# Performance work log

Measured on AMD Instinct MI355X. Metric: run time of the kernel, lower is better.

The kernel has to match this reference:

```python
import jax, jax.numpy as jnp
import numpy as np

N_BITS = 8
IN_F = 4096
OUT_F = 1024
THRESHOLD = 0.5


def _ripple_accumulate(bits, n_bits):
    # bits: [N, I, n_bits], little-endian bit vectors (last bit is the sign bit).
    # Sequentially add each of the I bit-vectors into an accumulator via
    # ripple-carry binary addition (straight-through gradients on the carry).
    N = bits.shape[0]
    dt = bits.dtype

    def add_step(acc, x):  # acc, x: [N, n_bits]
        carry = jnp.zeros((N,), dt)
        outs = []
        for b in range(n_bits):
            s = acc[:, b] + x[:, b] + carry
            carry = jax.lax.stop_gradient(jnp.floor(s * 0.5))
            outs.append(s - 2.0 * carry)  # s mod 2, STE through the floor
        return jnp.stack(outs, axis=-1), None

    acc0 = jnp.zeros((N, n_bits), dt)
    acc, _ = jax.lax.scan(add_step, acc0, jnp.swapaxes(bits, 0, 1))  # scan over I
    return acc


def residual_adder(features, weights, true_sum, n_bits):
    # features/weights/true_sum: [N, I, n_bits]. Ripple-carry accumulate the
    # filtered feature bits per neuron, return the bitwise residual vs the
    # target sum bits (trigger signal).
    acc = _ripple_accumulate(features, n_bits)  # [N, n_bits]
    return acc - true_sum[:, 0, :]


def setup_inputs() -> dict:
    key = jax.random.key(0)
    k1, k2, k3 = jax.random.split(key, 3)
    latent = jax.random.uniform(k1, (1, IN_F), dtype=jnp.float32)
    true_sum = jax.random.randint(k2, (1, OUT_F * N_BITS), 0, 2).astype(jnp.float32)
    weight = jax.random.uniform(k3, (IN_F, OUT_F * N_BITS), dtype=jnp.float32)
    return {"latent": latent, "true_sum": true_sum, "weight": weight}


def reference(latent, true_sum, weight):
    B = latent.shape[0]  # must be 1 (see torch repeat semantics)
    dt = weight.dtype
    # straight-through hard binarization of the weight
    hard = weight + jax.lax.stop_gradient((weight > THRESHOLD).astype(dt) - weight)
    powers = (2.0 ** jnp.arange(N_BITS, dtype=dt)).at[-1].multiply(-1.0)  # two's complement
    int_w = jax.lax.stop_gradient((hard.reshape(IN_F, OUT_F, N_BITS) * powers).sum(-1))  # [IN_F, OUT_F]
    int_s = jax.lax.stop_gradient((true_sum.reshape(B, OUT_F, N_BITS) * powers).sum(-1))  # [B, OUT_F]
    pred = latent @ int_w  # [B, OUT_F]
    loss = 0.5 * jnp.mean((pred - int_s) ** 2)
    # per-bit filtered features, regrouped per neuron
    filtered = jax.lax.stop_gradient(latent)[:, :, None] * hard[None]  # [B, IN_F, OUT_F*N_BITS]
    fbn = filtered.reshape(B, IN_F, OUT_F, N_BITS).transpose(0, 2, 1, 3).reshape(B * OUT_F, IN_F, N_BITS)
    # torch 2D .repeat(1, IN_F, 1) -> [1, B*IN_F, OUT_F*N_BITS]
    ts = jnp.tile(true_sum[None], (1, IN_F, 1))
    tbn = ts.reshape(1, B * IN_F, OUT_F, N_BITS).transpose(0, 2, 1, 3).reshape(OUT_F, B * IN_F, N_BITS)
    wbn = jnp.broadcast_to(weight[None], (B, IN_F, OUT_F * N_BITS)).reshape(B, IN_F, OUT_F, N_BITS).transpose(0, 2, 1, 3).reshape(B * OUT_F, IN_F, N_BITS)
    trigger = residual_adder(fbn, wbn, tbn, N_BITS)  # [B*OUT_F, N_BITS]
    return loss, trigger
```

## Files before the change

kernel.cpp:

```cpp
#include <hip/hip_runtime.h>
#include <cmath>

#define IN_F   4096
#define OUT_F  1024
#define NBITS  8
#define JTOT   (OUT_F * NBITS)
#define TB     256
#define CPT    4
#define JBLK   (TB * CPT)
#define NJB    (JTOT / JBLK)
#define ROWS   64
#define NCHUNK (IN_F / ROWS)

typedef float f32x4 __attribute__((ext_vector_type(4)));

__global__ __launch_bounds__(TB) void colsum_kernel(
    const float* __restrict__ w, const float* __restrict__ latent,
    float* __restrict__ partials, float* __restrict__ out) {
  const int j0 = (blockIdx.x * TB + threadIdx.x) * CPT;
  const int chunk = blockIdx.y;
  const int i0 = chunk * ROWS;
  if (blockIdx.x == 0 && blockIdx.y == 0 && threadIdx.x == 0) out[0] = 0.0f;

  float a0 = 0.f, a1 = 0.f, a2 = 0.f, a3 = 0.f;
  const f32x4* wp = reinterpret_cast<const f32x4*>(w + (size_t)i0 * JTOT + j0);
#pragma unroll 32
  for (int r = 0; r < ROWS; ++r) {
    const float lat = latent[i0 + r];
    const f32x4 v = __builtin_nontemporal_load(wp + (size_t)r * (JTOT / 4));
    a0 += (v.x > 0.5f) ? lat : 0.0f;
    a1 += (v.y > 0.5f) ? lat : 0.0f;
    a2 += (v.z > 0.5f) ? lat : 0.0f;
    a3 += (v.w > 0.5f) ? lat : 0.0f;
  }
  float* p = partials + (size_t)chunk * JTOT + j0;
  p[0] = a0; p[1] = a1; p[2] = a2; p[3] = a3;
}

__global__ __launch_bounds__(TB) void finalize_kernel(
    const float* __restrict__ partials, const float* __restrict__ true_sum,
    float* __restrict__ out) {
  const int tid = threadIdx.x;
  const int j = blockIdx.x * TB + tid;
  double s = 0.0;
#pragma unroll 8
  for (int c = 0; c < NCHUNK; ++c)
    s += (double)partials[(size_t)c * JTOT + j];

  __shared__ double S[TB];
  __shared__ double err[TB / NBITS];
  S[tid] = s;
  __syncthreads();

  if (tid < TB / NBITS) {
    const int o_local = tid;
    const int jbase = blockIdx.x * TB + o_local * NBITS;
    const double pw[NBITS] = {1.0, 2.0, 4.0, 8.0, 16.0, 32.0, 64.0, -128.0};
    double C = 0.0, pred = 0.0, ints = 0.0;
#pragma unroll
    for (int b = 0; b < NBITS; ++b) {
      const double Sb = S[o_local * NBITS + b];
      const double ts = (double)true_sum[jbase + b];
      const double T  = Sb + C;
      const double c2 = floor(T * 0.5);
      const double ab = T - 2.0 * c2;
      C = c2;
      out[1 + jbase + b] = (float)(ab - ts);
      pred += pw[b] * Sb;
      ints += pw[b] * ts;
    }
    const double d = pred - ints;
    err[o_local] = d * d;
  }
  __syncthreads();

  if (tid == 0) {
    double e = 0.0;
    for (int k = 0; k < TB / NBITS; ++k) e += err[k];
    atomicAdd(out, (float)(e * (0.5 / (double)OUT_F)));
  }
}

extern "C" void kernel_launch(void* const* d_in, const int* in_sizes, int n_in,
                              void* d_out, int out_size, void* d_ws, size_t ws_size,
                              hipStream_t stream) {
  const float* latent   = (const float*)d_in[0];
  const float* true_sum = (const float*)d_in[1];
  const float* w        = (const float*)d_in[2];
  float* out = (float*)d_out;
  float* partials = (float*)d_ws;

  colsum_kernel<<<dim3(NJB, NCHUNK), TB, 0, stream>>>(w, latent, partials, out);
  finalize_kernel<<<dim3(JTOT / TB), TB, 0, stream>>>(partials, true_sum, out);
}
```

Measured before the change: 192.6 us.

## Fuse column-sum and finalize into one kernel via last-block atomic counters

Merges the two kernels into one: each column block's chunk writes its partials, and the last chunk to finish (found with an atomic counter) reduces all partials for that column block and computes the ripple bits and the loss. A second counter lets the last finalizer sum the per-block losses deterministically instead of using a float atomicAdd. This removes one kernel launch and the gap between the launches, but adds a memset launch, threadfences, and a tail in which 8 blocks do the reduction serially.

```diff
diff --git a/kernel.cpp b/kernel.cpp
--- a/kernel.cpp
+++ b/kernel.cpp
@@ -11,16 +11,20 @@
 #define NJB    (JTOT / JBLK)
 #define ROWS   64
 #define NCHUNK (IN_F / ROWS)
+#define NEUR_PER_CB (JBLK / NBITS)
 
 typedef float f32x4 __attribute__((ext_vector_type(4)));
 
-__global__ __launch_bounds__(TB) void colsum_kernel(
+__global__ __launch_bounds__(TB) void fused_kernel(
     const float* __restrict__ w, const float* __restrict__ latent,
-    float* __restrict__ partials, float* __restrict__ out) {
-  const int j0 = (blockIdx.x * TB + threadIdx.x) * CPT;
+    const float* __restrict__ true_sum, float* __restrict__ partials,
+    double* __restrict__ lossp, int* __restrict__ ctr,
+    int* __restrict__ fin_ctr, float* __restrict__ out) {
+  const int x = blockIdx.x;
   const int chunk = blockIdx.y;
+  const int tid = threadIdx.x;
+  const int j0 = x * JBLK + tid * CPT;
   const int i0 = chunk * ROWS;
-  if (blockIdx.x == 0 && blockIdx.y == 0 && threadIdx.x == 0) out[0] = 0.0f;
 
   float a0 = 0.f, a1 = 0.f, a2 = 0.f, a3 = 0.f;
   const f32x4* wp = reinterpret_cast<const f32x4*>(w + (size_t)i0 * JTOT + j0);
@@ -33,51 +37,65 @@
     a2 += (v.z > 0.5f) ? lat : 0.0f;
     a3 += (v.w > 0.5f) ? lat : 0.0f;
   }
-  float* p = partials + (size_t)chunk * JTOT + j0;
-  p[0] = a0; p[1] = a1; p[2] = a2; p[3] = a3;
-}
+  f32x4 acc = {a0, a1, a2, a3};
+  *reinterpret_cast<f32x4*>(partials + (size_t)chunk * JTOT + j0) = acc;
 
-__global__ __launch_bounds__(TB) void finalize_kernel(
-    const float* __restrict__ partials, const float* __restrict__ true_sum,
-    float* __restrict__ out) {
-  const int tid = threadIdx.x;
-  const int j = blockIdx.x * TB + tid;
-  double s = 0.0;
+  __threadfence();
+  __syncthreads();
+  __shared__ int is_last;
+  if (tid == 0)
+    is_last = (atomicAdd(ctr + x, 1) == NCHUNK - 1) ? 1 : 0;
+  __syncthreads();
+  if (!is_last) return;
+  __threadfence();
+
+  double s0 = 0.0, s1 = 0.0, s2 = 0.0, s3 = 0.0;
+  const float* pp = partials + j0;
 #pragma unroll 8
-  for (int c = 0; c < NCHUNK; ++c)
-    s += (double)partials[(size_t)c * JTOT + j];
-
-  __shared__ double S[TB];
-  __shared__ double err[TB / NBITS];
-  S[tid] = s;
+  for (int c = 0; c < NCHUNK; ++c) {
+    const f32x4 v = *reinterpret_cast<const f32x4*>(pp + (size_t)c * JTOT);
+    s0 += (double)v.x; s1 += (double)v.y; s2 += (double)v.z; s3 += (double)v.w;
+  }
+  __shared__ double S[JBLK];
+  S[tid * 4 + 0] = s0; S[tid * 4 + 1] = s1;
+  S[tid * 4 + 2] = s2; S[tid * 4 + 3] = s3;
   __syncthreads();
 
-  if (tid < TB / NBITS) {
-    const int o_local = tid;
-    const int jbase = blockIdx.x * TB + o_local * NBITS;
+  __shared__ double err[NEUR_PER_CB];
+  if (tid < NEUR_PER_CB) {
+    const int jloc = tid * NBITS;
+    const int jglob = x * JBLK + jloc;
     const double pw[NBITS] = {1.0, 2.0, 4.0, 8.0, 16.0, 32.0, 64.0, -128.0};
     double C = 0.0, pred = 0.0, ints = 0.0;
 #pragma unroll
     for (int b = 0; b < NBITS; ++b) {
-      const double Sb = S[o_local * NBITS + b];
-      const double ts = (double)true_sum[jbase + b];
+      const double Sb = S[jloc + b];
+      const double ts = (double)true_sum[jglob + b];
       const double T  = Sb + C;
       const double c2 = floor(T * 0.5);
-      const double ab = T - 2.0 * c2;
       C = c2;
-      out[1 + jbase + b] = (float)(ab - ts);
+      out[1 + jglob + b] = (float)((T - 2.0 * c2) - ts);
       pred += pw[b] * Sb;
       ints += pw[b] * ts;
     }
     const double d = pred - ints;
-    err[o_local] = d * d;
+    err[tid] = d * d;
   }
   __syncthreads();
 
   if (tid == 0) {
     double e = 0.0;
-    for (int k = 0; k < TB / NBITS; ++k) e += err[k];
-    atomicAdd(out, (float)(e * (0.5 / (double)OUT_F)));
+#pragma unroll 16
+    for (int k = 0; k < NEUR_PER_CB; ++k) e += err[k];
+    lossp[x] = e;
+    __threadfence();
+    if (atomicAdd(fin_ctr, 1) == NJB - 1) {
+      __threadfence();
+      double t = 0.0;
+#pragma unroll
+      for (int k = 0; k < NJB; ++k) t += lossp[k];
+      out[0] = (float)(t * (0.5 / (double)OUT_F));
+    }
   }
 }
 
@@ -88,8 +106,13 @@
   const float* true_sum = (const float*)d_in[1];
   const float* w        = (const float*)d_in[2];
   float* out = (float*)d_out;
-  float* partials = (float*)d_ws;
 
-  colsum_kernel<<<dim3(NJB, NCHUNK), TB, 0, stream>>>(w, latent, partials, out);
-  finalize_kernel<<<dim3(JTOT / TB), TB, 0, stream>>>(partials, true_sum, out);
+  float*  partials = (float*)d_ws;
+  double* lossp    = (double*)(partials + (size_t)NCHUNK * JTOT);
+  int*    ctr      = (int*)(lossp + NJB);
+  int*    fin_ctr  = ctr + NJB;
+
+  hipMemsetAsync(ctr, 0, (NJB + 1) * sizeof(int), stream);
+  fused_kernel<<<dim3(NJB, NCHUNK), TB, 0, stream>>>(
+      w, latent, true_sum, partials, lossp, ctr, fin_ctr, out);
 }
```

Measured after the change: 269.3 us. +39.8%, slower.
